# Kernel optimization log

Hardware: AMD Instinct MI355X
Metric: run time of the kernel (lower is better)

## Reference

```python
import jax, jax.numpy as jnp
import numpy as np

# Standard icosahedron face list (20 faces over 12 vertices).
ICO_FACES = np.array([
    [0, 11, 5], [0, 5, 1], [0, 1, 7], [0, 7, 10], [0, 10, 11],
    [1, 5, 9], [5, 11, 4], [11, 10, 2], [10, 7, 6], [7, 1, 8],
    [3, 9, 4], [3, 4, 2], [3, 2, 6], [3, 6, 8], [3, 8, 9],
    [4, 9, 5], [2, 4, 11], [6, 2, 10], [8, 6, 7], [9, 8, 1],
], dtype=np.int64)


def _ico_face_adjacency():
    # Faces are adjacent iff they share an edge == share exactly 2 vertices.
    adj = np.zeros((20, 20), dtype=np.float32)
    for i in range(20):
        for j in range(i + 1, 20):
            if len(set(ICO_FACES[i]) & set(ICO_FACES[j])) == 2:
                adj[i, j] = adj[j, i] = 1.0
    return jnp.asarray(adj)


def setup_inputs() -> dict:
    key = jax.random.key(0)
    ks = jax.random.split(key, 9)
    B, D = 65536, 512
    def w(k, fan_in, fan_out):
        return jax.random.normal(k, (fan_in, fan_out), jnp.float32) * (1.0 / np.sqrt(fan_in))
    return {
        "z": jax.random.normal(ks[0], (B, D), jnp.float32),
        "W1": w(ks[1], D, 512), "b1": jnp.zeros((512,), jnp.float32),
        "W2": w(ks[2], 512, 256), "b2": jnp.zeros((256,), jnp.float32),
        "W3": w(ks[3], 256, 128), "b3": jnp.zeros((128,), jnp.float32),
        "W4": w(ks[4], 128, 20), "b4": jnp.zeros((20,), jnp.float32),
        "precomputed_adj": _ico_face_adjacency(),  # [20,20], zero diagonal
    }


def reference(z, W1, b1, W2, b2, W3, b3, W4, b4, precomputed_adj):
    # Eval path: dropout = identity, recon_loss = 0.
    h = jax.nn.relu(z @ W1 + b1)
    h = jax.nn.relu(h @ W2 + b2)
    h = jax.nn.relu(h @ W3 + b3)
    face_probs = jax.nn.sigmoid(h @ W4 + b4)          # [B, 20]
    face_mask = (face_probs > 0.5).astype(z.dtype)    # [B, 20]
    # outer(mask, mask) * precomputed adjacency; diagonal of adj is already 0,
    # reproducing the i != j condition of the original triple loop.
    adj_matrix = face_mask[:, :, None] * face_mask[:, None, :] * precomputed_adj  # [B,20,20]
    recon_loss = jnp.asarray(0.0, jnp.float32)
    return (adj_matrix, face_mask, face_probs, recon_loss)
```

## Files before the change

### kernel.cpp

```cpp
#include <hip/hip_runtime.h>
#include <math.h>

#define NT   1024
#define BR   32
#define TAU  1e-3f
#define LIST_CAP 65536

typedef _Float16 half8 __attribute__((ext_vector_type(8)));
typedef float    f32x4 __attribute__((ext_vector_type(4)));
typedef unsigned int u32x4 __attribute__((ext_vector_type(4)));

#define SWZ(r) (((r)&7)<<4)

#define PACK_ELS 425984
#define OFF_LIST 16
#define OFF_PH   (16 + LIST_CAP*4)
#define OFF_PL   (OFF_PH + PACK_ELS*2)
#define WS_PACK_NEED (OFF_PL + PACK_ELS*2)
#define WS_F32_NEED  (16 + LIST_CAP*4)

__device__ __forceinline__ int p1(int c){ return ((c&7)<<6)|(c>>3); }
__device__ __forceinline__ int p2(int c){ return ((c&3)<<6)|(c>>2); }
__device__ __forceinline__ int p3(int c){ return ((c&1)<<6)|(c>>1); }

__global__ void pack_w(const float* __restrict__ W1, const float* __restrict__ W2,
                       const float* __restrict__ W3,
                       _Float16* __restrict__ PH, _Float16* __restrict__ PL) {
    int i = blockIdx.x * 256 + threadIdx.x;
    if (i >= PACK_ELS) return;
    const float* W; int N, KS, loc;
    if (i < 262144)            { W = W1; N = 512; KS = 16; loc = i; }
    else if (i < 393216)       { W = W2; N = 256; KS = 16; loc = i - 262144; }
    else                       { W = W3; N = 128; KS = 8;  loc = i - 393216; }
    int j   = loc & 7;
    int l   = (loc >> 3) & 63;
    int rest = loc >> 9;
    int ks  = rest & (KS - 1);
    int nt  = rest >> (KS == 16 ? 4 : 3);
    int k = ks * 32 + (l >> 4) * 8 + j;
    int n = nt * 16 + (l & 15);
    float v = W[k * N + n];
    _Float16 hi = (_Float16)v;
    _Float16 lo = (_Float16)(v - (float)hi);
    PH[i] = hi; PL[i] = lo;
}

__device__ __forceinline__ u32x4 agl(const _Float16* p) {
    u32x4 d;
    asm volatile("global_load_dwordx4 %0, %1, off" : "=v"(d) : "v"(p));
    return d;
}
template<int NWAIT> __device__ __forceinline__ void waitv() {
    if constexpr (NWAIT == 0)      asm volatile("s_waitcnt vmcnt(0)");
    else if constexpr (NWAIT == 2) asm volatile("s_waitcnt vmcnt(2)");
    else if constexpr (NWAIT == 4) asm volatile("s_waitcnt vmcnt(4)");
    else                           asm volatile("s_waitcnt vmcnt(8)");
    __builtin_amdgcn_sched_barrier(0);
}

template<int K, int N, int NTW, int MREP, bool SPLIT_OUT>
__device__ __forceinline__ void mfma_layer(const char* __restrict__ actIn,
    const _Float16* __restrict__ PH, const _Float16* __restrict__ PL,
    const float* __restrict__ bias,
    char* __restrict__ actOut, float* __restrict__ h3out,
    int nt0, int m0, int l)
{
    constexpr int KS    = K / 32;
    constexpr int BATCH = 2 * NTW;
    const int r  = l & 15;
    const int kg = l >> 4;
    f32x4 acc[MREP][NTW];
#pragma unroll
    for (int t = 0; t < NTW; ++t) {
        float bb = bias[(nt0 + t) * 16 + r];
#pragma unroll
        for (int m = 0; m < MREP; ++m) acc[m][t] = (f32x4){bb, bb, bb, bb};
    }
    __builtin_amdgcn_sched_barrier(0);
    constexpr int loIn = BR * K * 2;

#define AADDR(m, ks) ((((((m0 + (m)) * 16 + r) * K + kg * 8 + (ks) * 32) * 2) ^ SWZ((m0 + (m)) * 16 + r)))
#define BOFF(t, ks)  (((size_t)((nt0 + (t)) * KS + (ks)) * 64 + l) * 8)

    u32x4 Bh[3][NTW], Bl[3][NTW];
#pragma unroll
    for (int t = 0; t < NTW; ++t) { Bh[0][t] = agl(PH + BOFF(t, 0)); Bl[0][t] = agl(PL + BOFF(t, 0)); }
#pragma unroll
    for (int t = 0; t < NTW; ++t) { Bh[1][t] = agl(PH + BOFF(t, 1)); Bl[1][t] = agl(PL + BOFF(t, 1)); }

#pragma unroll
    for (int ks = 0; ks < KS; ++ks) {
        const int cur = ks % 3, nx = (ks + 2) % 3;
        if (ks + 2 < KS) {
#pragma unroll
            for (int t = 0; t < NTW; ++t) {
                Bh[nx][t] = agl(PH + BOFF(t, ks + 2));
                Bl[nx][t] = agl(PL + BOFF(t, ks + 2));
            }
        }
        half8 ah[MREP], al[MREP];
#pragma unroll
        for (int m = 0; m < MREP; ++m) {
            int ao = AADDR(m, ks);
            ah[m] = *(const half8*)(actIn + ao);
            al[m] = *(const half8*)(actIn + ao + loIn);
        }
        const int rem = KS - 1 - ks;
        if (rem >= 2)      waitv<2 * BATCH>();
        else if (rem == 1) waitv<BATCH>();
        else               waitv<0>();
        __builtin_amdgcn_s_setprio(1);
#pragma unroll
        for (int t = 0; t < NTW; ++t) {
            half8 bh = __builtin_bit_cast(half8, Bh[cur][t]);
            half8 bl = __builtin_bit_cast(half8, Bl[cur][t]);
#pragma unroll
            for (int m = 0; m < MREP; ++m) {
                acc[m][t] = __builtin_amdgcn_mfma_f32_16x16x32_f16(ah[m], bh, acc[m][t], 0, 0, 0);
                acc[m][t] = __builtin_amdgcn_mfma_f32_16x16x32_f16(ah[m], bl, acc[m][t], 0, 0, 0);
                acc[m][t] = __builtin_amdgcn_mfma_f32_16x16x32_f16(al[m], bh, acc[m][t], 0, 0, 0);
            }
        }
        __builtin_amdgcn_s_setprio(0);
        __builtin_amdgcn_sched_barrier(0);
    }
#undef AADDR
#undef BOFF

    constexpr int loOut = BR * N * 2;
#pragma unroll
    for (int t = 0; t < NTW; ++t) {
        int n = (nt0 + t) * 16 + r;
#pragma unroll
        for (int m = 0; m < MREP; ++m)
#pragma unroll
        for (int b = 0; b < 4; ++b) {
            int rowD = (m0 + m) * 16 + kg * 4 + b;
            float v = acc[m][t][b];
            v = v > 0.f ? v : 0.f;
            if constexpr (SPLIT_OUT) {
                _Float16 hi = (_Float16)v;
                _Float16 lo = (_Float16)(v - (float)hi);
                int lin = (rowD * N + n) * 2;
                int sw  = lin ^ SWZ(rowD);
                *(_Float16*)(actOut + sw)         = hi;
                *(_Float16*)(actOut + sw + loOut) = lo;
            } else {
                h3out[rowD * 132 + n] = v;
            }
        }
    }
}

__global__ __launch_bounds__(NT, 4)
void dec_mfma(const float* __restrict__ z,
              const float* __restrict__ b1, const float* __restrict__ b2,
              const float* __restrict__ b3,
              const float* __restrict__ W4, const float* __restrict__ b4,
              const float* __restrict__ adj,
              const _Float16* __restrict__ PH, const _Float16* __restrict__ PL,
              float* __restrict__ out, int B,
              int* __restrict__ cnt, int* __restrict__ list)
{
    __shared__ __align__(16) char ldsA[65536];
    __shared__ __align__(16) char ldsB[65536];
    __shared__ float logitsS[BR * 20];
    __shared__ float maskS[BR * 20];
    __shared__ float adjS[400];

    const int tid = threadIdx.x;
    const int w   = tid >> 6;
    const int l   = tid & 63;
    const int rowBase = blockIdx.x * BR;

    const int O_MASK  = B * 400;
    const int O_PROBS = O_MASK + B * 20;
    const int O_LOSS  = O_PROBS + B * 20;

    if (tid < 400) adjS[tid] = adj[tid];

    {
        int r   = tid >> 5;
        int c16 = (tid & 31) * 16;
        const float4* zp = (const float4*)(z + (size_t)(rowBase + r) * 512 + c16);
        float4 f0 = zp[0], f1 = zp[1], f2 = zp[2], f3 = zp[3];
        float fv[16] = {f0.x,f0.y,f0.z,f0.w, f1.x,f1.y,f1.z,f1.w,
                        f2.x,f2.y,f2.z,f2.w, f3.x,f3.y,f3.z,f3.w};
        half8 hi0, hi1, lo0, lo1;
#pragma unroll
        for (int j = 0; j < 8; ++j) {
            _Float16 h = (_Float16)fv[j];
            hi0[j] = h; lo0[j] = (_Float16)(fv[j] - (float)h);
        }
#pragma unroll
        for (int j = 0; j < 8; ++j) {
            _Float16 h = (_Float16)fv[8 + j];
            hi1[j] = h; lo1[j] = (_Float16)(fv[8 + j] - (float)h);
        }
        int lin = (r * 512 + c16) * 2;
        int swz = SWZ(r);
        *(half8*)(ldsA + ((lin     ) ^ swz))          = hi0;
        *(half8*)(ldsA + ((lin + 16) ^ swz))          = hi1;
        *(half8*)(ldsA + ((lin     ) ^ swz) + 32768)  = lo0;
        *(half8*)(ldsA + ((lin + 16) ^ swz) + 32768)  = lo1;
    }
    __syncthreads();

    mfma_layer<512, 512, 2, 2, true >(ldsA, PH,          PL,          b1, ldsB, nullptr, w * 2, 0, l);
    __syncthreads();
    mfma_layer<512, 256, 1, 2, true >(ldsB, PH + 262144, PL + 262144, b2, ldsA, nullptr, w, 0, l);
    __syncthreads();
    mfma_layer<256, 128, 1, 1, false>(ldsA, PH + 393216, PL + 393216, b3, nullptr, (float*)ldsB, w & 7, w >> 3, l);
    __syncthreads();

    const float* h3 = (const float*)ldsB;
    for (int o = tid; o < BR * 20; o += NT) {
        int r = o / 20, c = o - r * 20;
        float acc = b4[c];
        for (int k = 0; k < 128; ++k)
            acc += h3[r * 132 + k] * W4[k * 20 + c];
        logitsS[o] = acc;
    }
    __syncthreads();

    if (tid < BR) {
        float mn = 1e30f;
#pragma unroll
        for (int c = 0; c < 20; ++c)
            mn = fminf(mn, fabsf(logitsS[tid * 20 + c]));
        if (mn < TAU) {
            int idx = atomicAdd(cnt, 1);
            if (idx < LIST_CAP) list[idx] = rowBase + tid;
        }
    }

    for (int o = tid; o < BR * 20; o += NT) {
        double lg = (double)logitsS[o];
        double p  = 1.0 / (1.0 + exp(-lg));
        out[O_PROBS + rowBase * 20 + o] = (float)p;
        float m = lg > 0.0 ? 1.0f : 0.0f;
        out[O_MASK + rowBase * 20 + o] = m;
        maskS[o] = m;
    }
    __syncthreads();

    for (int o = tid; o < BR * 20; o += NT) {
        int r = o / 20, ii = o - r * 20;
        float mri = maskS[r * 20 + ii];
        float* orow = &out[(rowBase + r) * 400 + ii * 20];
#pragma unroll
        for (int b = 0; b < 5; ++b) {
            float4 v;
            v.x = mri * maskS[r * 20 + 4*b+0] * adjS[ii * 20 + 4*b+0];
            v.y = mri * maskS[r * 20 + 4*b+1] * adjS[ii * 20 + 4*b+1];
            v.z = mri * maskS[r * 20 + 4*b+2] * adjS[ii * 20 + 4*b+2];
            v.w = mri * maskS[r * 20 + 4*b+3] * adjS[ii * 20 + 4*b+3];
            *(float4*)&orow[4*b] = v;
        }
    }

    if (blockIdx.x == 0 && tid == 0) out[O_LOSS] = 0.0f;
}

template<typename T, bool FLAG>
__global__ __launch_bounds__(256, 2)
void dec_fused(const float* __restrict__ z,
               const float* __restrict__ W1, const float* __restrict__ b1,
               const float* __restrict__ W2, const float* __restrict__ b2,
               const float* __restrict__ W3, const float* __restrict__ b3,
               const float* __restrict__ W4, const float* __restrict__ b4,
               const float* __restrict__ adj,
               float* __restrict__ out, int B,
               int* __restrict__ cnt, int* __restrict__ list)
{
    constexpr int STR = (sizeof(T) == 4) ? 20 : 17;
    __shared__ T     hT[512 * STR];
    __shared__ T     logitsS[16 * 20];
    __shared__ float maskS[16 * 20];
    __shared__ float adjS[400];

    const int tid = threadIdx.x;
    const int rg  = tid >> 6;
    const int cg  = tid & 63;
    const int r0  = rg * 4;
    const int rowBase = blockIdx.x * 16;

    const int O_MASK  = B * 400;
    const int O_PROBS = O_MASK + B * 20;
    const int O_LOSS  = O_PROBS + B * 20;

    for (int i = tid; i < 400; i += 256) adjS[i] = adj[i];
    for (int i = tid; i < 512 * 16; i += 256) {
        int k = i & 511, r = i >> 9;
        hT[k * STR + r] = (T)z[(rowBase + r) * 512 + k];
    }
    __syncthreads();
    {
        T a[4][8];
#pragma unroll
        for (int ri = 0; ri < 4; ++ri)
#pragma unroll
            for (int ci = 0; ci < 8; ++ci) a[ri][ci] = (T)0;
#pragma unroll 2
        for (int k = 0; k < 512; ++k) {
            T zr[4];
#pragma unroll
            for (int ri = 0; ri < 4; ++ri) zr[ri] = hT[k * STR + r0 + ri];
            const float4* w1p = (const float4*)(W1 + k * 512 + cg * 8);
            float4 w0 = w1p[0], w1v = w1p[1];
            T wv[8] = {(T)w0.x,(T)w0.y,(T)w0.z,(T)w0.w,
                       (T)w1v.x,(T)w1v.y,(T)w1v.z,(T)w1v.w};
#pragma unroll
            for (int ci = 0; ci < 8; ++ci)
#pragma unroll
                for (int ri = 0; ri < 4; ++ri)
                    a[ri][ci] += zr[ri] * wv[ci];
        }
        __syncthreads();
#pragma unroll
        for (int ci = 0; ci < 8; ++ci) {
            int c = cg * 8 + ci;
            T bb = (T)b1[c]; int cp = p1(c);
#pragma unroll
            for (int ri = 0; ri < 4; ++ri) {
                T v = a[ri][ci] + bb;
                hT[cp * STR + r0 + ri] = v > (T)0 ? v : (T)0;
            }
        }
        __syncthreads();
    }
    {
        T a[4][4];
#pragma unroll
        for (int ri = 0; ri < 4; ++ri)
#pragma unroll
            for (int ci = 0; ci < 4; ++ci) a[ri][ci] = (T)0;
#pragma unroll 2
        for (int k = 0; k < 512; ++k) {
            int kp = p1(k);
            T zr[4];
#pragma unroll
            for (int ri = 0; ri < 4; ++ri) zr[ri] = hT[kp * STR + r0 + ri];
            float4 wq = *(const float4*)(W2 + k * 256 + cg * 4);
            T wv[4] = {(T)wq.x,(T)wq.y,(T)wq.z,(T)wq.w};
#pragma unroll
            for (int ci = 0; ci < 4; ++ci)
#pragma unroll
                for (int ri = 0; ri < 4; ++ri)
                    a[ri][ci] += zr[ri] * wv[ci];
        }
        __syncthreads();
#pragma unroll
        for (int ci = 0; ci < 4; ++ci) {
            int c = cg * 4 + ci;
            T bb = (T)b2[c]; int cp = p2(c);
#pragma unroll
            for (int ri = 0; ri < 4; ++ri) {
                T v = a[ri][ci] + bb;
                hT[cp * STR + r0 + ri] = v > (T)0 ? v : (T)0;
            }
        }
        __syncthreads();
    }
    {
        T a[4][2];
#pragma unroll
        for (int ri = 0; ri < 4; ++ri)
#pragma unroll
            for (int ci = 0; ci < 2; ++ci) a[ri][ci] = (T)0;
#pragma unroll 2
        for (int k = 0; k < 256; ++k) {
            int kp = p2(k);
            T zr[4];
#pragma unroll
            for (int ri = 0; ri < 4; ++ri) zr[ri] = hT[kp * STR + r0 + ri];
            float2 wq = *(const float2*)(W3 + k * 128 + cg * 2);
            T wv[2] = {(T)wq.x,(T)wq.y};
#pragma unroll
            for (int ci = 0; ci < 2; ++ci)
#pragma unroll
                for (int ri = 0; ri < 4; ++ri)
                    a[ri][ci] += zr[ri] * wv[ci];
        }
        __syncthreads();
#pragma unroll
        for (int ci = 0; ci < 2; ++ci) {
            int c = cg * 2 + ci;
            T bb = (T)b3[c]; int cp = p3(c);
#pragma unroll
            for (int ri = 0; ri < 4; ++ri) {
                T v = a[ri][ci] + bb;
                hT[cp * STR + r0 + ri] = v > (T)0 ? v : (T)0;
            }
        }
        __syncthreads();
    }
    for (int o = tid; o < 16 * 20; o += 256) {
        int r = o / 20, c = o - r * 20;
        T acc = (T)b4[c];
        for (int k = 0; k < 128; ++k)
            acc += hT[p3(k) * STR + r] * (T)W4[k * 20 + c];
        logitsS[o] = acc;
    }
    __syncthreads();
    if constexpr (FLAG) {
        if (tid < 16) {
            float mn = 1e30f;
#pragma unroll
            for (int c = 0; c < 20; ++c)
                mn = fminf(mn, fabsf((float)logitsS[tid * 20 + c]));
            if (mn < TAU) {
                int idx = atomicAdd(cnt, 1);
                if (idx < LIST_CAP) list[idx] = rowBase + tid;
            }
        }
    }
    for (int o = tid; o < 16 * 20; o += 256) {
        double lg = (double)logitsS[o];
        double p  = 1.0 / (1.0 + exp(-lg));
        out[O_PROBS + rowBase * 20 + o] = (float)p;
        float m = lg > 0.0 ? 1.0f : 0.0f;
        out[O_MASK + rowBase * 20 + o] = m;
        maskS[o] = m;
    }
    __syncthreads();
    for (int o = tid; o < 16 * 20; o += 256) {
        int r = o / 20, ii = o - r * 20;
        float mri = maskS[r * 20 + ii];
        float* orow = &out[(rowBase + r) * 400 + ii * 20];
#pragma unroll
        for (int b = 0; b < 5; ++b) {
            float4 v;
            v.x = mri * maskS[r * 20 + 4*b+0] * adjS[ii * 20 + 4*b+0];
            v.y = mri * maskS[r * 20 + 4*b+1] * adjS[ii * 20 + 4*b+1];
            v.z = mri * maskS[r * 20 + 4*b+2] * adjS[ii * 20 + 4*b+2];
            v.w = mri * maskS[r * 20 + 4*b+3] * adjS[ii * 20 + 4*b+3];
            *(float4*)&orow[4*b] = v;
        }
    }
    if (blockIdx.x == 0 && tid == 0) out[O_LOSS] = 0.0f;
}

__global__ __launch_bounds__(256, 4)
void repair_rows(const float* __restrict__ z,
                 const float* __restrict__ W1, const float* __restrict__ b1,
                 const float* __restrict__ W2, const float* __restrict__ b2,
                 const float* __restrict__ W3, const float* __restrict__ b3,
                 const float* __restrict__ W4, const float* __restrict__ b4,
                 const float* __restrict__ adj,
                 float* __restrict__ out, int B,
                 const int* __restrict__ cnt, const int* __restrict__ list)
{
    __shared__ double bufA[512];
    __shared__ double bufB[512];
    __shared__ double lgS[20];
    __shared__ float  mskS[20];

    const int tid = threadIdx.x;
    const int O_MASK  = B * 400;
    const int O_PROBS = O_MASK + B * 20;

    int n = *cnt;
    if (n > LIST_CAP) n = LIST_CAP;

    for (int i = blockIdx.x; i < n; i += gridDim.x) {
        int row = list[i];
        for (int k = tid; k < 512; k += 256)
            bufA[k] = (double)z[(size_t)row * 512 + k];
        __syncthreads();
        {
            int c0 = tid, c1 = tid + 256;
            double a0 = (double)b1[c0], a1 = (double)b1[c1];
            for (int k = 0; k < 512; ++k) {
                double h = bufA[k];
                a0 += h * (double)W1[k * 512 + c0];
                a1 += h * (double)W1[k * 512 + c1];
            }
            __syncthreads();
            bufB[c0] = a0 > 0.0 ? a0 : 0.0;
            bufB[c1] = a1 > 0.0 ? a1 : 0.0;
            __syncthreads();
        }
        {
            double a0 = (double)b2[tid < 256 ? tid : 0];
            if (tid < 256)
                for (int k = 0; k < 512; ++k)
                    a0 += bufB[k] * (double)W2[k * 256 + tid];
            __syncthreads();
            if (tid < 256) bufA[tid] = a0 > 0.0 ? a0 : 0.0;
            __syncthreads();
        }
        {
            double a0 = (double)b3[tid < 128 ? tid : 0];
            if (tid < 128)
                for (int k = 0; k < 256; ++k)
                    a0 += bufA[k] * (double)W3[k * 128 + tid];
            __syncthreads();
            if (tid < 128) bufB[tid] = a0 > 0.0 ? a0 : 0.0;
            __syncthreads();
        }
        if (tid < 20) {
            double a0 = (double)b4[tid];
            for (int k = 0; k < 128; ++k)
                a0 += bufB[k] * (double)W4[k * 20 + tid];
            lgS[tid] = a0;
        }
        __syncthreads();
        if (tid < 20) {
            double lg = lgS[tid];
            out[O_PROBS + (size_t)row * 20 + tid] = (float)(1.0 / (1.0 + exp(-lg)));
            float m = lg > 0.0 ? 1.0f : 0.0f;
            out[O_MASK + (size_t)row * 20 + tid] = m;
            mskS[tid] = m;
        }
        __syncthreads();
        for (int o = tid; o < 400; o += 256) {
            int ii = o / 20, jj = o - ii * 20;
            out[(size_t)row * 400 + o] = mskS[ii] * mskS[jj] * adj[o];
        }
        __syncthreads();
    }
}

extern "C" void kernel_launch(void* const* d_in, const int* in_sizes, int n_in,
                              void* d_out, int out_size, void* d_ws, size_t ws_size,
                              hipStream_t stream) {
    const float* z   = (const float*)d_in[0];
    const float* W1  = (const float*)d_in[1];
    const float* b1  = (const float*)d_in[2];
    const float* W2  = (const float*)d_in[3];
    const float* b2  = (const float*)d_in[4];
    const float* W3  = (const float*)d_in[5];
    const float* b3  = (const float*)d_in[6];
    const float* W4  = (const float*)d_in[7];
    const float* b4  = (const float*)d_in[8];
    const float* adj = (const float*)d_in[9];
    float* out = (float*)d_out;

    const int B = in_sizes[0] / 512;

    if (ws_size >= (size_t)WS_PACK_NEED) {
        int* cnt  = (int*)d_ws;
        int* list = (int*)((char*)d_ws + OFF_LIST);
        _Float16* PH = (_Float16*)((char*)d_ws + OFF_PH);
        _Float16* PL = (_Float16*)((char*)d_ws + OFF_PL);
        hipMemsetAsync(d_ws, 0, 16, stream);
        hipLaunchKernelGGL(pack_w, dim3((PACK_ELS + 255) / 256), dim3(256), 0, stream,
                           W1, W2, W3, PH, PL);
        hipLaunchKernelGGL(dec_mfma, dim3(B / BR), dim3(NT), 0, stream,
                           z, b1, b2, b3, W4, b4, adj, PH, PL, out, B, cnt, list);
        hipLaunchKernelGGL(repair_rows, dim3(1024), dim3(256), 0, stream,
                           z, W1, b1, W2, b2, W3, b3, W4, b4, adj, out, B, cnt, list);
    } else if (ws_size >= (size_t)WS_F32_NEED) {
        int* cnt  = (int*)d_ws;
        int* list = (int*)((char*)d_ws + OFF_LIST);
        hipMemsetAsync(d_ws, 0, 16, stream);
        hipLaunchKernelGGL((dec_fused<float, true>), dim3(B / 16), dim3(256), 0, stream,
                           z, W1, b1, W2, b2, W3, b3, W4, b4, adj, out, B, cnt, list);
        hipLaunchKernelGGL(repair_rows, dim3(1024), dim3(256), 0, stream,
                           z, W1, b1, W2, b2, W3, b3, W4, b4, adj, out, B, cnt, list);
    } else {
        hipLaunchKernelGGL((dec_fused<double, false>), dim3(B / 16), dim3(256), 0, stream,
                           z, W1, b1, W2, b2, W3, b3, W4, b4, adj, out, B,
                           (int*)nullptr, (int*)nullptr);
    }
}
```

Measured before the change: 446.8 us.

## Halve block threads, widen per-wave tiles, deepen B prefetch and prefetch A

Cuts the block from 1024 to 512 threads, so each wave computes twice as many output tiles (NTW doubled, or MREP doubled in layer 3). This means each A fragment read from LDS feeds more MFMAs. The global prefetch of packed weights goes from 2 to 3 stages ahead, and the A fragments for the next k-step are loaded from LDS while the current step's MFMAs run. The z staging loop now strides so the smaller block still covers all rows. The cost is higher register pressure (launch bounds lowered to 2 blocks per CU), which reduces occupancy, and each block issues fewer memory requests in parallel.

```diff
diff --git a/kernel.cpp b/kernel.cpp
--- a/kernel.cpp
+++ b/kernel.cpp
@@ -1,7 +1,7 @@
 #include <hip/hip_runtime.h>
 #include <math.h>
 
-#define NT   1024
+#define NT   512
 #define BR   32
 #define TAU  1e-3f
 #define LIST_CAP 65536
@@ -51,10 +51,14 @@
     return d;
 }
 template<int NWAIT> __device__ __forceinline__ void waitv() {
-    if constexpr (NWAIT == 0)      asm volatile("s_waitcnt vmcnt(0)");
-    else if constexpr (NWAIT == 2) asm volatile("s_waitcnt vmcnt(2)");
-    else if constexpr (NWAIT == 4) asm volatile("s_waitcnt vmcnt(4)");
-    else                           asm volatile("s_waitcnt vmcnt(8)");
+    if constexpr (NWAIT == 0)       asm volatile("s_waitcnt vmcnt(0)");
+    else if constexpr (NWAIT == 2)  asm volatile("s_waitcnt vmcnt(2)");
+    else if constexpr (NWAIT == 4)  asm volatile("s_waitcnt vmcnt(4)");
+    else if constexpr (NWAIT == 6)  asm volatile("s_waitcnt vmcnt(6)");
+    else if constexpr (NWAIT == 8)  asm volatile("s_waitcnt vmcnt(8)");
+    else if constexpr (NWAIT == 12) asm volatile("s_waitcnt vmcnt(12)");
+    else if constexpr (NWAIT == 16) asm volatile("s_waitcnt vmcnt(16)");
+    else                            asm volatile("s_waitcnt vmcnt(24)");
     __builtin_amdgcn_sched_barrier(0);
 }
 
@@ -82,31 +86,47 @@
 #define AADDR(m, ks) ((((((m0 + (m)) * 16 + r) * K + kg * 8 + (ks) * 32) * 2) ^ SWZ((m0 + (m)) * 16 + r)))
 #define BOFF(t, ks)  (((size_t)((nt0 + (t)) * KS + (ks)) * 64 + l) * 8)
 
-    u32x4 Bh[3][NTW], Bl[3][NTW];
-#pragma unroll
-    for (int t = 0; t < NTW; ++t) { Bh[0][t] = agl(PH + BOFF(t, 0)); Bl[0][t] = agl(PL + BOFF(t, 0)); }
-#pragma unroll
-    for (int t = 0; t < NTW; ++t) { Bh[1][t] = agl(PH + BOFF(t, 1)); Bl[1][t] = agl(PL + BOFF(t, 1)); }
+    u32x4 Bh[4][NTW], Bl[4][NTW];
+#pragma unroll
+    for (int p = 0; p < 3; ++p) {
+        if (p < KS) {
+#pragma unroll
+            for (int t = 0; t < NTW; ++t) {
+                Bh[p][t] = agl(PH + BOFF(t, p));
+                Bl[p][t] = agl(PL + BOFF(t, p));
+            }
+        }
+    }
+    half8 ah0[MREP], al0[MREP];
+#pragma unroll
+    for (int m = 0; m < MREP; ++m) {
+        int ao = AADDR(m, 0);
+        ah0[m] = *(const half8*)(actIn + ao);
+        al0[m] = *(const half8*)(actIn + ao + loIn);
+    }
 
 #pragma unroll
     for (int ks = 0; ks < KS; ++ks) {
-        const int cur = ks % 3, nx = (ks + 2) % 3;
-        if (ks + 2 < KS) {
+        const int cur = ks & 3, nx = (ks + 3) & 3;
+        if (ks + 3 < KS) {
 #pragma unroll
             for (int t = 0; t < NTW; ++t) {
-                Bh[nx][t] = agl(PH + BOFF(t, ks + 2));
-                Bl[nx][t] = agl(PL + BOFF(t, ks + 2));
-            }
-        }
-        half8 ah[MREP], al[MREP];
-#pragma unroll
-        for (int m = 0; m < MREP; ++m) {
-            int ao = AADDR(m, ks);
-            ah[m] = *(const half8*)(actIn + ao);
-            al[m] = *(const half8*)(actIn + ao + loIn);
+                Bh[nx][t] = agl(PH + BOFF(t, ks + 3));
+                Bl[nx][t] = agl(PL + BOFF(t, ks + 3));
+            }
+        }
+        half8 ahn[MREP], aln[MREP];
+        if (ks + 1 < KS) {
+#pragma unroll
+            for (int m = 0; m < MREP; ++m) {
+                int ao = AADDR(m, ks + 1);
+                ahn[m] = *(const half8*)(actIn + ao);
+                aln[m] = *(const half8*)(actIn + ao + loIn);
+            }
         }
         const int rem = KS - 1 - ks;
-        if (rem >= 2)      waitv<2 * BATCH>();
+        if (rem >= 3)      waitv<3 * BATCH>();
+        else if (rem == 2) waitv<2 * BATCH>();
         else if (rem == 1) waitv<BATCH>();
         else               waitv<0>();
         __builtin_amdgcn_s_setprio(1);
@@ -116,13 +136,15 @@
             half8 bl = __builtin_bit_cast(half8, Bl[cur][t]);
 #pragma unroll
             for (int m = 0; m < MREP; ++m) {
-                acc[m][t] = __builtin_amdgcn_mfma_f32_16x16x32_f16(ah[m], bh, acc[m][t], 0, 0, 0);
-                acc[m][t] = __builtin_amdgcn_mfma_f32_16x16x32_f16(ah[m], bl, acc[m][t], 0, 0, 0);
-                acc[m][t] = __builtin_amdgcn_mfma_f32_16x16x32_f16(al[m], bh, acc[m][t], 0, 0, 0);
+                acc[m][t] = __builtin_amdgcn_mfma_f32_16x16x32_f16(ah0[m], bh, acc[m][t], 0, 0, 0);
+                acc[m][t] = __builtin_amdgcn_mfma_f32_16x16x32_f16(ah0[m], bl, acc[m][t], 0, 0, 0);
+                acc[m][t] = __builtin_amdgcn_mfma_f32_16x16x32_f16(al0[m], bh, acc[m][t], 0, 0, 0);
             }
         }
         __builtin_amdgcn_s_setprio(0);
         __builtin_amdgcn_sched_barrier(0);
+#pragma unroll
+        for (int m = 0; m < MREP; ++m) { ah0[m] = ahn[m]; al0[m] = aln[m]; }
     }
 #undef AADDR
 #undef BOFF
@@ -152,7 +174,7 @@
     }
 }
 
-__global__ __launch_bounds__(NT, 4)
+__global__ __launch_bounds__(NT, 2)
 void dec_mfma(const float* __restrict__ z,
               const float* __restrict__ b1, const float* __restrict__ b2,
               const float* __restrict__ b3,
@@ -179,9 +201,10 @@
 
     if (tid < 400) adjS[tid] = adj[tid];
 
-    {
-        int r   = tid >> 5;
-        int c16 = (tid & 31) * 16;
+#pragma unroll
+    for (int i = tid; i < BR * 32; i += NT) {
+        int r   = i >> 5;
+        int c16 = (i & 31) * 16;
         const float4* zp = (const float4*)(z + (size_t)(rowBase + r) * 512 + c16);
         float4 f0 = zp[0], f1 = zp[1], f2 = zp[2], f3 = zp[3];
         float fv[16] = {f0.x,f0.y,f0.z,f0.w, f1.x,f1.y,f1.z,f1.w,
@@ -206,11 +229,11 @@
     }
     __syncthreads();
 
-    mfma_layer<512, 512, 2, 2, true >(ldsA, PH,          PL,          b1, ldsB, nullptr, w * 2, 0, l);
-    __syncthreads();
-    mfma_layer<512, 256, 1, 2, true >(ldsB, PH + 262144, PL + 262144, b2, ldsA, nullptr, w, 0, l);
-    __syncthreads();
-    mfma_layer<256, 128, 1, 1, false>(ldsA, PH + 393216, PL + 393216, b3, nullptr, (float*)ldsB, w & 7, w >> 3, l);
+    mfma_layer<512, 512, 4, 2, true >(ldsA, PH,          PL,          b1, ldsB, nullptr, w * 4, 0, l);
+    __syncthreads();
+    mfma_layer<512, 256, 2, 2, true >(ldsB, PH + 262144, PL + 262144, b2, ldsA, nullptr, w * 2, 0, l);
+    __syncthreads();
+    mfma_layer<256, 128, 1, 2, false>(ldsA, PH + 393216, PL + 393216, b3, nullptr, (float*)ldsB, w, 0, l);
     __syncthreads();
 
     const float* h3 = (const float*)ldsB;
```

Measured after the change: 456.5 us. 2.2% more time.

## Batch repair rows per block, transpose W4, and use fast float sigmoid

Applied to the files above, without the earlier changes.

The fp64 repair kernel now handles 8 flagged rows per block, so each W1/W2/W3 weight load is reused across those rows instead of being reloaded for every row. The pack kernel also writes a transposed W4 and zeroes the counter, which removes the separate memset launch and lets the layer-4 dot product read W4 with float4 vector loads. The main kernel computes the sigmoid in float with __expf instead of double exp. In exchange the repair kernel uses more registers and LDS (launch bounds lowered to 2 blocks), and the float sigmoid may differ slightly in the last bits of the probabilities.

```diff
diff --git a/kernel.cpp b/kernel.cpp
--- a/kernel.cpp
+++ b/kernel.cpp
@@ -5,6 +5,7 @@
 #define BR   32
 #define TAU  1e-3f
 #define LIST_CAP 65536
+#define RPB  8
 
 typedef _Float16 half8 __attribute__((ext_vector_type(8)));
 typedef float    f32x4 __attribute__((ext_vector_type(4)));
@@ -16,7 +17,8 @@
 #define OFF_LIST 16
 #define OFF_PH   (16 + LIST_CAP*4)
 #define OFF_PL   (OFF_PH + PACK_ELS*2)
-#define WS_PACK_NEED (OFF_PL + PACK_ELS*2)
+#define OFF_W4T  (OFF_PL + PACK_ELS*2)
+#define WS_PACK_NEED (OFF_W4T + 2560*4)
 #define WS_F32_NEED  (16 + LIST_CAP*4)
 
 __device__ __forceinline__ int p1(int c){ return ((c&7)<<6)|(c>>3); }
@@ -24,10 +26,19 @@
 __device__ __forceinline__ int p3(int c){ return ((c&1)<<6)|(c>>1); }
 
 __global__ void pack_w(const float* __restrict__ W1, const float* __restrict__ W2,
-                       const float* __restrict__ W3,
-                       _Float16* __restrict__ PH, _Float16* __restrict__ PL) {
+                       const float* __restrict__ W3, const float* __restrict__ W4,
+                       _Float16* __restrict__ PH, _Float16* __restrict__ PL,
+                       float* __restrict__ W4T, int* __restrict__ cnt) {
     int i = blockIdx.x * 256 + threadIdx.x;
-    if (i >= PACK_ELS) return;
+    if (i == 0) *cnt = 0;
+    if (i >= PACK_ELS) {
+        int t = i - PACK_ELS;
+        if (t < 2560) {
+            int c = t >> 7, k = t & 127;
+            W4T[c * 128 + k] = W4[k * 20 + c];
+        }
+        return;
+    }
     const float* W; int N, KS, loc;
     if (i < 262144)            { W = W1; N = 512; KS = 16; loc = i; }
     else if (i < 393216)       { W = W2; N = 256; KS = 16; loc = i - 262144; }
@@ -156,7 +167,7 @@
 void dec_mfma(const float* __restrict__ z,
               const float* __restrict__ b1, const float* __restrict__ b2,
               const float* __restrict__ b3,
-              const float* __restrict__ W4, const float* __restrict__ b4,
+              const float* __restrict__ W4T, const float* __restrict__ b4,
               const float* __restrict__ adj,
               const _Float16* __restrict__ PH, const _Float16* __restrict__ PL,
               float* __restrict__ out, int B,
@@ -216,10 +227,16 @@
     const float* h3 = (const float*)ldsB;
     for (int o = tid; o < BR * 20; o += NT) {
         int r = o / 20, c = o - r * 20;
-        float acc = b4[c];
-        for (int k = 0; k < 128; ++k)
-            acc += h3[r * 132 + k] * W4[k * 20 + c];
-        logitsS[o] = acc;
+        const float4* hp = (const float4*)(h3 + r * 132);
+        const float4* wp = (const float4*)(W4T + c * 128);
+        f32x4 av = (f32x4){0.f, 0.f, 0.f, 0.f};
+#pragma unroll
+        for (int kk = 0; kk < 32; ++kk) {
+            float4 h = hp[kk], wv = wp[kk];
+            av[0] += h.x * wv.x; av[1] += h.y * wv.y;
+            av[2] += h.z * wv.z; av[3] += h.w * wv.w;
+        }
+        logitsS[o] = b4[c] + ((av[0] + av[1]) + (av[2] + av[3]));
     }
     __syncthreads();
 
@@ -235,10 +252,9 @@
     }
 
     for (int o = tid; o < BR * 20; o += NT) {
-        double lg = (double)logitsS[o];
-        double p  = 1.0 / (1.0 + exp(-lg));
-        out[O_PROBS + rowBase * 20 + o] = (float)p;
-        float m = lg > 0.0 ? 1.0f : 0.0f;
+        float lg = logitsS[o];
+        out[O_PROBS + rowBase * 20 + o] = 1.0f / (1.0f + __expf(-lg));
+        float m = lg > 0.0f ? 1.0f : 0.0f;
         out[O_MASK + rowBase * 20 + o] = m;
         maskS[o] = m;
     }
@@ -441,7 +457,7 @@
     if (blockIdx.x == 0 && tid == 0) out[O_LOSS] = 0.0f;
 }
 
-__global__ __launch_bounds__(256, 4)
+__global__ __launch_bounds__(256, 2)
 void repair_rows(const float* __restrict__ z,
                  const float* __restrict__ W1, const float* __restrict__ b1,
                  const float* __restrict__ W2, const float* __restrict__ b2,
@@ -451,10 +467,10 @@
                  float* __restrict__ out, int B,
                  const int* __restrict__ cnt, const int* __restrict__ list)
 {
-    __shared__ double bufA[512];
-    __shared__ double bufB[512];
-    __shared__ double lgS[20];
-    __shared__ float  mskS[20];
+    __shared__ double zA[RPB][512];
+    __shared__ double hB[RPB][512];
+    __shared__ double lgS[RPB][20];
+    __shared__ float  mskS[RPB][20];
 
     const int tid = threadIdx.x;
     const int O_MASK  = B * 400;
@@ -462,61 +478,110 @@
 
     int n = *cnt;
     if (n > LIST_CAP) n = LIST_CAP;
-
-    for (int i = blockIdx.x; i < n; i += gridDim.x) {
-        int row = list[i];
-        for (int k = tid; k < 512; k += 256)
-            bufA[k] = (double)z[(size_t)row * 512 + k];
-        __syncthreads();
+    int nbatch = (n + RPB - 1) / RPB;
+
+    for (int g = blockIdx.x; g < nbatch; g += gridDim.x) {
+        int nv = n - g * RPB; if (nv > RPB) nv = RPB;
+        int rows[RPB];
+#pragma unroll
+        for (int j = 0; j < RPB; ++j)
+            rows[j] = list[g * RPB + (j < nv ? j : 0)];
+
+        for (int i = tid; i < RPB * 512; i += 256) {
+            int j = i >> 9, k = i & 511;
+            zA[j][k] = (double)z[(size_t)rows[j] * 512 + k];
+        }
+        __syncthreads();
+
         {
             int c0 = tid, c1 = tid + 256;
-            double a0 = (double)b1[c0], a1 = (double)b1[c1];
+            double a0[RPB], a1[RPB];
+#pragma unroll
+            for (int j = 0; j < RPB; ++j) { a0[j] = (double)b1[c0]; a1[j] = (double)b1[c1]; }
             for (int k = 0; k < 512; ++k) {
-                double h = bufA[k];
-                a0 += h * (double)W1[k * 512 + c0];
-                a1 += h * (double)W1[k * 512 + c1];
+                double w0 = (double)W1[k * 512 + c0];
+                double w1 = (double)W1[k * 512 + c1];
+#pragma unroll
+                for (int j = 0; j < RPB; ++j) {
+                    double h = zA[j][k];
+                    a0[j] += h * w0;
+                    a1[j] += h * w1;
+                }
             }
             __syncthreads();
-            bufB[c0] = a0 > 0.0 ? a0 : 0.0;
-            bufB[c1] = a1 > 0.0 ? a1 : 0.0;
+#pragma unroll
+            for (int j = 0; j < RPB; ++j) {
+                hB[j][c0] = a0[j] > 0.0 ? a0[j] : 0.0;
+                hB[j][c1] = a1[j] > 0.0 ? a1[j] : 0.0;
+            }
             __syncthreads();
         }
         {
-            double a0 = (double)b2[tid < 256 ? tid : 0];
-            if (tid < 256)
-                for (int k = 0; k < 512; ++k)
-                    a0 += bufB[k] * (double)W2[k * 256 + tid];
+            double a0[RPB];
+#pragma unroll
+            for (int j = 0; j < RPB; ++j) a0[j] = (double)b2[tid < 256 ? tid : 0];
+            if (tid < 256) {
+                for (int k = 0; k < 512; ++k) {
+                    double wv = (double)W2[k * 256 + tid];
+#pragma unroll
+                    for (int j = 0; j < RPB; ++j) a0[j] += hB[j][k] * wv;
+                }
+            }
             __syncthreads();
-            if (tid < 256) bufA[tid] = a0 > 0.0 ? a0 : 0.0;
+            if (tid < 256) {
+#pragma unroll
+                for (int j = 0; j < RPB; ++j)
+                    zA[j][tid] = a0[j] > 0.0 ? a0[j] : 0.0;
+            }
             __syncthreads();
         }
         {
-            double a0 = (double)b3[tid < 128 ? tid : 0];
-            if (tid < 128)
-                for (int k = 0; k < 256; ++k)
-                    a0 += bufA[k] * (double)W3[k * 128 + tid];
+            double a0[RPB];
+#pragma unroll
+            for (int j = 0; j < RPB; ++j) a0[j] = (double)b3[tid < 128 ? tid : 0];
+            if (tid < 128) {
+                for (int k = 0; k < 256; ++k) {
+                    double wv = (double)W3[k * 128 + tid];
+#pragma unroll
+                    for (int j = 0; j < RPB; ++j) a0[j] += zA[j][k] * wv;
+                }
+            }
             __syncthreads();
-            if (tid < 128) bufB[tid] = a0 > 0.0 ? a0 : 0.0;
+            if (tid < 128) {
+#pragma unroll
+                for (int j = 0; j < RPB; ++j)
+                    hB[j][tid] = a0[j] > 0.0 ? a0[j] : 0.0;
+            }
             __syncthreads();
         }
-        if (tid < 20) {
-            double a0 = (double)b4[tid];
+        if (tid < RPB * 20) {
+            int j = tid / 20, c = tid - j * 20;
+            double a0 = (double)b4[c];
             for (int k = 0; k < 128; ++k)
-                a0 += bufB[k] * (double)W4[k * 20 + tid];
-            lgS[tid] = a0;
-        }
-        __syncthreads();
-        if (tid < 20) {
-            double lg = lgS[tid];
-            out[O_PROBS + (size_t)row * 20 + tid] = (float)(1.0 / (1.0 + exp(-lg)));
+                a0 += hB[j][k] * (double)W4[k * 20 + c];
+            lgS[j][c] = a0;
+        }
+        __syncthreads();
+
+        if (tid < RPB * 20) {
+            int j = tid / 20, c = tid - j * 20;
+            double lg = lgS[j][c];
             float m = lg > 0.0 ? 1.0f : 0.0f;
-            out[O_MASK + (size_t)row * 20 + tid] = m;
-            mskS[tid] = m;
-        }
-        __syncthreads();
-        for (int o = tid; o < 400; o += 256) {
-            int ii = o / 20, jj = o - ii * 20;
-            out[(size_t)row * 400 + o] = mskS[ii] * mskS[jj] * adj[o];
+            mskS[j][c] = m;
+            if (j < nv) {
+                size_t row = (size_t)rows[j];
+                out[O_PROBS + row * 20 + c] = (float)(1.0 / (1.0 + exp(-lg)));
+                out[O_MASK + row * 20 + c] = m;
+            }
+        }
+        __syncthreads();
+
+        for (int i = tid; i < RPB * 400; i += 256) {
+            int j = i / 400, e = i - j * 400;
+            if (j < nv) {
+                int ii = e / 20, jj = e - ii * 20;
+                out[(size_t)rows[j] * 400 + e] = mskS[j][ii] * mskS[j][jj] * adj[e];
+            }
         }
         __syncthreads();
     }
@@ -544,12 +609,12 @@
         int* list = (int*)((char*)d_ws + OFF_LIST);
         _Float16* PH = (_Float16*)((char*)d_ws + OFF_PH);
         _Float16* PL = (_Float16*)((char*)d_ws + OFF_PL);
-        hipMemsetAsync(d_ws, 0, 16, stream);
-        hipLaunchKernelGGL(pack_w, dim3((PACK_ELS + 255) / 256), dim3(256), 0, stream,
-                           W1, W2, W3, PH, PL);
+        float* W4T = (float*)((char*)d_ws + OFF_W4T);
+        hipLaunchKernelGGL(pack_w, dim3((PACK_ELS + 2560 + 255) / 256), dim3(256), 0, stream,
+                           W1, W2, W3, W4, PH, PL, W4T, cnt);
         hipLaunchKernelGGL(dec_mfma, dim3(B / BR), dim3(NT), 0, stream,
-                           z, b1, b2, b3, W4, b4, adj, PH, PL, out, B, cnt, list);
-        hipLaunchKernelGGL(repair_rows, dim3(1024), dim3(256), 0, stream,
+                           z, b1, b2, b3, W4T, b4, adj, PH, PL, out, B, cnt, list);
+        hipLaunchKernelGGL(repair_rows, dim3(512), dim3(256), 0, stream,
                            z, W1, b1, W2, b2, W3, b3, W4, b4, adj, out, B, cnt, list);
     } else if (ws_size >= (size_t)WS_F32_NEED) {
         int* cnt  = (int*)d_ws;
@@ -557,7 +622,7 @@
         hipMemsetAsync(d_ws, 0, 16, stream);
         hipLaunchKernelGGL((dec_fused<float, true>), dim3(B / 16), dim3(256), 0, stream,
                            z, W1, b1, W2, b2, W3, b3, W4, b4, adj, out, B, cnt, list);
-        hipLaunchKernelGGL(repair_rows, dim3(1024), dim3(256), 0, stream,
+        hipLaunchKernelGGL(repair_rows, dim3(512), dim3(256), 0, stream,
                            z, W1, b1, W2, b2, W3, b3, W4, b4, adj, out, B, cnt, list);
     } else {
         hipLaunchKernelGGL((dec_fused<double, false>), dim3(B / 16), dim3(256), 0, stream,
```

Result: faster. 424.6 us (median of 2 runs) (-5.0%).
